# Kernel optimization log

Hardware: AMD Instinct MI355X
Metric: run time of the kernel (lower is better)

The kernel has to match this reference:

```python
import jax, jax.numpy as jnp
import numpy as np

B, T, D, H = 4, 2048, 1024, 16

def setup_inputs() -> dict:
    key = jax.random.key(0)
    ks = jax.random.split(key, 5)
    s = 1.0 / np.sqrt(D)
    return {
        "x":  jax.random.normal(ks[0], (B, T, D), dtype=jnp.float32),
        "Wq": jax.random.uniform(ks[1], (D, D), jnp.float32, -s, s),
        "Wk": jax.random.uniform(ks[2], (D, D), jnp.float32, -s, s),
        "Wv": jax.random.uniform(ks[3], (D, D), jnp.float32, -s, s),
        "Wo": jax.random.uniform(ks[4], (D, D), jnp.float32, -s, s),
    }

def reference(x, Wq, Wk, Wv, Wo):
    Bv, Tv, Dv = x.shape
    h = H
    k = Dv // h
    # Linear (no bias): y = x @ W.T, then split heads -> [B, h, T, k]
    Q = (x @ Wq.T).reshape(Bv, Tv, h, k).transpose(0, 2, 1, 3)
    K = (x @ Wk.T).reshape(Bv, Tv, h, k).transpose(0, 2, 1, 3)
    V = (x @ Wv.T).reshape(Bv, Tv, h, k).transpose(0, 2, 1, 3)
    scores = jnp.einsum('bhqk,bhsk->bhqs', Q, K) / jnp.sqrt(jnp.asarray(k, x.dtype))
    causal = jnp.tril(jnp.ones((Tv, Tv), dtype=bool))
    scores = jnp.where(causal[None, None], scores, jnp.asarray(-jnp.inf, x.dtype))
    A = jax.nn.softmax(scores, axis=-1)
    Y = jnp.einsum('bhqs,bhsk->bhqk', A, V).transpose(0, 2, 1, 3).reshape(Bv, Tv, Dv)
    return Y @ Wo.T
```

## Files before the change

kernel.cpp:

```cpp
#include <hip/hip_runtime.h>

typedef __attribute__((ext_vector_type(8))) short short8;
typedef __attribute__((ext_vector_type(4))) float f32x4;
typedef __attribute__((ext_vector_type(2))) unsigned int u32x2;

constexpr int B_ = 4, T_ = 2048, D_ = 1024, H_ = 16;
constexpr int M_ = B_ * T_;
constexpr float SCL2 = 0.1803368801111f;

#if __has_builtin(__builtin_amdgcn_exp2f)
#define EXP2F __builtin_amdgcn_exp2f
#else
#define EXP2F exp2f
#endif

#define DEV __device__ __forceinline__

DEV unsigned short f2bf(float f) {
  unsigned int u = __builtin_bit_cast(unsigned int, f);
  u += 0x7FFFu + ((u >> 16) & 1u);
  return (unsigned short)(u >> 16);
}

DEV void gload16(const unsigned short* g, unsigned short* l) {
  __builtin_amdgcn_global_load_lds(
      (const __attribute__((address_space(1))) unsigned int*)g,
      (__attribute__((address_space(3))) unsigned int*)l, 16, 0, 0);
}

__global__ __launch_bounds__(256) void cvt_bf16(const float* __restrict__ in,
                                                unsigned short* __restrict__ out,
                                                int n) {
  int i = (blockIdx.x * 256 + threadIdx.x) * 4;
  if (i >= n) return;
  float4 f = *(const float4*)(in + i);
  ushort4 o;
  o.x = f2bf(f.x); o.y = f2bf(f.y); o.z = f2bf(f.z); o.w = f2bf(f.w);
  *(ushort4*)(out + i) = o;
}

__global__ __launch_bounds__(256) void cvt_w4(const float* __restrict__ w0, const float* __restrict__ w1,
                                              const float* __restrict__ w2, const float* __restrict__ w3,
                                              unsigned short* __restrict__ o0, unsigned short* __restrict__ o1,
                                              unsigned short* __restrict__ o2, unsigned short* __restrict__ o3) {
  int sel = blockIdx.x >> 10;
  const float* in = sel == 0 ? w0 : sel == 1 ? w1 : sel == 2 ? w2 : w3;
  unsigned short* out = sel == 0 ? o0 : sel == 1 ? o1 : sel == 2 ? o2 : o3;
  int i = ((blockIdx.x & 1023) * 256 + threadIdx.x) * 4;
  float4 f = *(const float4*)(in + i);
  ushort4 o;
  o.x = f2bf(f.x); o.y = f2bf(f.y); o.z = f2bf(f.z); o.w = f2bf(f.w);
  *(ushort4*)(out + i) = o;
}

template <int OUTMODE>
__global__ __launch_bounds__(256, 2) void gemm_bt(const unsigned short* __restrict__ A,
                                                  const unsigned short* __restrict__ B,
                                                  void* __restrict__ C,
                                                  int M, int N, int K) {
  constexpr int BM = 128, BN = 128, BK = 64;
  __shared__ __align__(16) unsigned short a_sh[2 * BM * BK];
  __shared__ __align__(16) unsigned short b_sh[2 * BN * BK];

  const int tid = threadIdx.x;
  const int lane = tid & 63;
  const int w = tid >> 6;
  const int l15 = lane & 15, lg = lane >> 4;
  const int wr = w >> 1, wc = w & 1;

  const int nwg = gridDim.x;
  const int swz = (blockIdx.x & 7) * (nwg >> 3) + (blockIdx.x >> 3);

  const int NT = N / BN;
  const int tm = swz / NT, tn = swz % NT;
  const unsigned short* Ab = A + (size_t)tm * BM * K;
  const unsigned short* Bb = B + (size_t)tn * BN * K;

  f32x4 acc[4][4];
#pragma unroll
  for (int m = 0; m < 4; ++m)
#pragma unroll
    for (int n = 0; n < 4; ++n) acc[m][n] = (f32x4){0.f, 0.f, 0.f, 0.f};

  auto stage = [&](int buf, int kt) {
    int k0 = kt * BK;
#pragma unroll
    for (int rnd = 0; rnd < 4; ++rnd) {
      int c = rnd * 256 + tid;
      int row = c >> 3, s = c & 7;
      int koff = k0 + 8 * (s ^ (row & 7));
      unsigned short* ldst_a = a_sh + buf * BM * BK + (rnd * 256 + w * 64) * 8;
      unsigned short* ldst_b = b_sh + buf * BN * BK + (rnd * 256 + w * 64) * 8;
      gload16(Ab + (size_t)row * K + koff, ldst_a);
      gload16(Bb + (size_t)row * K + koff, ldst_b);
    }
  };

  stage(0, 0);
  int cur = 0;
  const int NK = K / BK;
  for (int kt = 0; kt < NK; ++kt) {
    __syncthreads();
    if (kt + 1 < NK) stage(cur ^ 1, kt + 1);
    const unsigned short* ab = a_sh + cur * BM * BK;
    const unsigned short* bb = b_sh + cur * BN * BK;
#pragma unroll
    for (int kk = 0; kk < 2; ++kk) {
      short8 af[4], bf8[4];
#pragma unroll
      for (int m = 0; m < 4; ++m) {
        int row = wr * 64 + m * 16 + l15;
        int slot = (kk * 4 + lg) ^ (row & 7);
        af[m] = *(const short8*)(ab + row * 64 + slot * 8);
      }
#pragma unroll
      for (int n = 0; n < 4; ++n) {
        int row = wc * 64 + n * 16 + l15;
        int slot = (kk * 4 + lg) ^ (row & 7);
        bf8[n] = *(const short8*)(bb + row * 64 + slot * 8);
      }
#pragma unroll
      for (int m = 0; m < 4; ++m)
#pragma unroll
        for (int n = 0; n < 4; ++n)
          acc[m][n] = __builtin_amdgcn_mfma_f32_16x16x32_bf16(af[m], bf8[n], acc[m][n], 0, 0, 0);
    }
    cur ^= 1;
  }

  const int row0 = tm * BM + wr * 64 + lg * 4;
  const int col0 = tn * BN + wc * 64 + l15;
#pragma unroll
  for (int m = 0; m < 4; ++m)
#pragma unroll
    for (int n = 0; n < 4; ++n) {
      if (OUTMODE == 3) {
        const int region = tn >> 3;
        const int nc = col0 - (region << 10) + n * 16;
        const int mm = row0 + m * 16;
        if (region == 2) {
          size_t base = (size_t)2 * 8388608 +
                        ((size_t)((mm >> 11) * 16 + (nc >> 6))) * 131072 +
                        (size_t)(nc & 63) * 2048 + (mm & 2047);
          ushort4 pk;
          pk.x = f2bf(acc[m][n][0]); pk.y = f2bf(acc[m][n][1]);
          pk.z = f2bf(acc[m][n][2]); pk.w = f2bf(acc[m][n][3]);
          *(ushort4*)((unsigned short*)C + base) = pk;
        } else {
          unsigned short* dst = (unsigned short*)C + (size_t)region * 8388608;
#pragma unroll
          for (int r = 0; r < 4; ++r)
            dst[(size_t)(mm + r) * 1024 + nc] = f2bf(acc[m][n][r]);
        }
      } else {
#pragma unroll
        for (int r = 0; r < 4; ++r) {
          size_t idx = (size_t)(row0 + m * 16 + r) * N + (col0 + n * 16);
          if (OUTMODE == 1)
            ((float*)C)[idx] = acc[m][n][r];
          else
            ((unsigned short*)C)[idx] = f2bf(acc[m][n][r]);
        }
      }
    }
}

__global__ __launch_bounds__(256, 3) void attn(const unsigned short* __restrict__ Q,
                                               const unsigned short* __restrict__ K,
                                               const unsigned short* __restrict__ Vt,
                                               unsigned short* __restrict__ Y) {
  __shared__ __align__(16) unsigned short k_sh[2][64 * 64];
  __shared__ __align__(16) unsigned short v_sh[2][64 * 64];
  __shared__ __align__(16) unsigned short p_sh[4][32][72];

  const int tid = threadIdx.x;
  const int lane = tid & 63;
  const int w = tid >> 6;
  const int l15 = lane & 15, lg = lane >> 4;

  const int bid = blockIdx.x;
  const int qt_blk = 15 - (bid >> 6);
  const int bh = bid & 63;
  const int h = bh & 15;
  const int b = bh >> 4;
  const int q0 = qt_blk * 128;
  const int qq0 = q0 + 32 * w;

  const unsigned short* Qp = Q + ((size_t)(b * T_ + q0)) * D_ + h * 64;
  const unsigned short* Kp = K + ((size_t)(b * T_)) * D_ + h * 64;
  const unsigned short* Vtp = Vt + (size_t)bh * 131072;

  auto stK = [&](int buf, int kv0) {
#pragma unroll
    for (int j = 0; j < 2; ++j) {
      int c = j * 256 + tid;
      int row = c >> 3;
      gload16(Kp + (size_t)(kv0 + row) * D_ + 8 * ((c & 7) ^ (row & 7)),
              &k_sh[buf][(j * 256 + w * 64) * 8]);
    }
  };
  auto stV = [&](int buf, int kv0) {
#pragma unroll
    for (int j = 0; j < 2; ++j) {
      int c = j * 256 + tid;
      int d = c >> 3;
      gload16(Vtp + (size_t)d * 2048 + kv0 + 8 * ((c & 7) ^ (d & 7)),
              &v_sh[buf][(j * 256 + w * 64) * 8]);
    }
  };

  short8 qf[2][2];
#pragma unroll
  for (int qt = 0; qt < 2; ++qt)
#pragma unroll
    for (int kk = 0; kk < 2; ++kk)
      qf[qt][kk] = *(const short8*)(Qp + (size_t)(32 * w + 16 * qt + l15) * D_ + 32 * kk + 8 * lg);

  stK(0, 0);
  stV(0, 0);
  __syncthreads();

  unsigned short* p_w = &p_sh[w][0][0];

  const float NEGINF = -__builtin_inff();
  float ml[2] = {NEGINF, NEGINF};
  float ll[2] = {0.f, 0.f};
  f32x4 o[2][4];
#pragma unroll
  for (int qt = 0; qt < 2; ++qt)
#pragma unroll
    for (int t = 0; t < 4; ++t) o[qt][t] = (f32x4){0.f, 0.f, 0.f, 0.f};

  const int NI = 2 * qt_blk + 2;
  int cur = 0;
  for (int i = 0; i < NI; ++i) {
    const int kv0 = i * 64;
    if (i + 1 < NI) { stK(cur ^ 1, kv0 + 64); stV(cur ^ 1, kv0 + 64); }

    const bool active = (kv0 <= qq0 + 31);
    if (active) {
      f32x4 sacc[2][4];
#pragma unroll
      for (int qt = 0; qt < 2; ++qt)
#pragma unroll
        for (int t = 0; t < 4; ++t) sacc[qt][t] = (f32x4){0.f, 0.f, 0.f, 0.f};
      const char* kb = (const char*)k_sh[cur];
      __builtin_amdgcn_s_setprio(1);
#pragma unroll
      for (int t = 0; t < 4; ++t) {
        int sr = 16 * t + l15;
        int sw = (sr & 7) << 4;
        short8 kf0 = *(const short8*)(kb + sr * 128 + ((16 * lg) ^ sw));
        short8 kf1 = *(const short8*)(kb + sr * 128 + ((64 + 16 * lg) ^ sw));
#pragma unroll
        for (int qt = 0; qt < 2; ++qt) {
          sacc[qt][t] = __builtin_amdgcn_mfma_f32_16x16x32_bf16(kf0, qf[qt][0], sacc[qt][t], 0, 0, 0);
          sacc[qt][t] = __builtin_amdgcn_mfma_f32_16x16x32_bf16(kf1, qf[qt][1], sacc[qt][t], 0, 0, 0);
        }
      }
      __builtin_amdgcn_s_setprio(0);

      float corr[2];
      bool defer[2];
#pragma unroll
      for (int qt = 0; qt < 2; ++qt) {
        const bool nomask = (kv0 + 63) <= (qq0 + 16 * qt);
        float sv[16];
        if (nomask) {
#pragma unroll
          for (int t = 0; t < 4; ++t)
#pragma unroll
            for (int r = 0; r < 4; ++r) sv[4 * t + r] = sacc[qt][t][r];
        } else {
          const int qg = qq0 + 16 * qt + l15;
#pragma unroll
          for (int t = 0; t < 4; ++t)
#pragma unroll
            for (int r = 0; r < 4; ++r) {
              int sg = kv0 + 16 * t + 4 * lg + r;
              sv[4 * t + r] = (sg <= qg) ? sacc[qt][t][r] : NEGINF;
            }
        }
        float a8[8], a4[4], a2[2];
#pragma unroll
        for (int k = 0; k < 8; ++k) a8[k] = fmaxf(sv[k], sv[k + 8]);
#pragma unroll
        for (int k = 0; k < 4; ++k) a4[k] = fmaxf(a8[k], a8[k + 4]);
        a2[0] = fmaxf(a4[0], a4[2]); a2[1] = fmaxf(a4[1], a4[3]);
        float mx = fmaxf(a2[0], a2[1]);
        mx = fmaxf(mx, __shfl_xor(mx, 16));
        mx = fmaxf(mx, __shfl_xor(mx, 32));
        defer[qt] = (__all(mx <= ml[qt] + 8.0f) != 0);
        float mnew = defer[qt] ? ml[qt] : fmaxf(ml[qt], mx);
        corr[qt] = defer[qt] ? 1.0f : EXP2F((ml[qt] - mnew) * SCL2);
        float nms2 = mnew * SCL2;
        float pv[16];
#pragma unroll
        for (int k = 0; k < 16; ++k) pv[k] = EXP2F(fmaf(sv[k], SCL2, -nms2));
        float s8[8], s4[4], s2[2];
#pragma unroll
        for (int k = 0; k < 8; ++k) s8[k] = pv[k] + pv[k + 8];
#pragma unroll
        for (int k = 0; k < 4; ++k) s4[k] = s8[k] + s8[k + 4];
        s2[0] = s4[0] + s4[2]; s2[1] = s4[1] + s4[3];
        float ps = s2[0] + s2[1];
        ps += __shfl_xor(ps, 16);
        ps += __shfl_xor(ps, 32);
        ll[qt] = ll[qt] * corr[qt] + ps;
        ml[qt] = mnew;
#pragma unroll
        for (int t = 0; t < 4; ++t) {
          unsigned lo, hi;
          asm("v_cvt_pk_bf16_f32 %0, %1, %2" : "=v"(lo) : "v"(pv[4 * t]), "v"(pv[4 * t + 1]));
          asm("v_cvt_pk_bf16_f32 %0, %1, %2" : "=v"(hi) : "v"(pv[4 * t + 2]), "v"(pv[4 * t + 3]));
          u32x2 pk = {lo, hi};
          *(u32x2*)(void*)(p_w + (16 * qt + l15) * 72 + 16 * t + 4 * lg) = pk;
        }
      }
      asm volatile("" ::: "memory");

#pragma unroll
      for (int qt = 0; qt < 2; ++qt)
        if (!defer[qt]) {
#pragma unroll
          for (int r = 0; r < 4; ++r) {
            float cr = __shfl(corr[qt], 4 * lg + r);
#pragma unroll
            for (int t = 0; t < 4; ++t) o[qt][t][r] *= cr;
          }
        }

      short8 pa[2][2];
#pragma unroll
      for (int qt = 0; qt < 2; ++qt)
#pragma unroll
        for (int kk = 0; kk < 2; ++kk)
          pa[qt][kk] = *(const short8*)(p_w + (16 * qt + l15) * 72 + kk * 32 + 8 * lg);

      const char* vbT = (const char*)v_sh[cur];
      __builtin_amdgcn_s_setprio(1);
#pragma unroll
      for (int t = 0; t < 4; ++t) {
        int dr = 16 * t + l15;
        int sw = (dr & 7) << 4;
        short8 vf0 = *(const short8*)(vbT + dr * 128 + ((16 * lg) ^ sw));
        short8 vf1 = *(const short8*)(vbT + dr * 128 + ((64 + 16 * lg) ^ sw));
#pragma unroll
        for (int qt = 0; qt < 2; ++qt) {
          o[qt][t] = __builtin_amdgcn_mfma_f32_16x16x32_bf16(pa[qt][0], vf0, o[qt][t], 0, 0, 0);
          o[qt][t] = __builtin_amdgcn_mfma_f32_16x16x32_bf16(pa[qt][1], vf1, o[qt][t], 0, 0, 0);
        }
      }
      __builtin_amdgcn_s_setprio(0);
    }
    __syncthreads();
    cur ^= 1;
  }

#pragma unroll
  for (int qt = 0; qt < 2; ++qt) {
    float linv = 1.0f / ll[qt];
#pragma unroll
    for (int r = 0; r < 4; ++r) {
      float li = __shfl(linv, 4 * lg + r);
      int qg = qq0 + 16 * qt + 4 * lg + r;
      unsigned short* Yp = Y + ((size_t)(b * T_ + qg)) * D_ + h * 64;
#pragma unroll
      for (int t = 0; t < 4; ++t)
        Yp[16 * t + l15] = f2bf(o[qt][t][r] * li);
    }
  }
}

extern "C" void kernel_launch(void* const* d_in, const int* in_sizes, int n_in,
                              void* d_out, int out_size, void* d_ws, size_t ws_size,
                              hipStream_t stream) {
  const float* x  = (const float*)d_in[0];
  const float* Wq = (const float*)d_in[1];
  const float* Wk = (const float*)d_in[2];
  const float* Wv = (const float*)d_in[3];
  const float* Wo = (const float*)d_in[4];
  float* out = (float*)d_out;

  const size_t NX = (size_t)M_ * D_;
  const size_t NW = (size_t)D_ * D_;
  const size_t need = (4 * NX + 4 * NW) * sizeof(unsigned short);
  if (ws_size < need) return;

  unsigned short* ws  = (unsigned short*)d_ws;
  unsigned short* xb  = ws;
  unsigned short* wqb = xb + NX;
  unsigned short* wkb = wqb + NW;
  unsigned short* wvb = wkb + NW;
  unsigned short* wob = wvb + NW;
  unsigned short* Qb  = wob + NW;
  unsigned short* Yb  = xb;

  cvt_bf16<<<(int)(NX / 1024), 256, 0, stream>>>(x, xb, (int)NX);
  cvt_w4<<<4096, 256, 0, stream>>>(Wq, Wk, Wv, Wo, wqb, wkb, wvb, wob);

  gemm_bt<3><<<(M_ / 128) * (3072 / 128), 256, 0, stream>>>(xb, wqb, Qb, M_, 3072, D_);

  attn<<<B_ * H_ * (T_ / 128), 256, 0, stream>>>(Qb, Qb + NX, Qb + 2 * NX, Yb);

  gemm_bt<1><<<(M_ / 128) * (D_ / 128), 256, 0, stream>>>(Yb, wob, out, M_, D_, D_);
}
```

Before: 167.2 us.

## Enlarge GEMM tile to 256x128 with 8 waves and ping-pong MFMA scheduling

The projection GEMMs move to a 256x128 tile computed by 512 threads (8 waves), with two K stages prefetched ahead and explicit vmcnt waits in place of a syncthreads before each stage. The MFMA work is split into four quadrant phases, each separated by s_barrier and setprio, so waves interleave LDS reads with matrix ops. The aim is more operand reuse per tile and better overlap of global loads with compute. In exchange it uses more LDS and registers per block, drops to one block per CU, and halves the grid size, so the tail and occupancy behaviour change.

```diff
diff --git a/kernel.cpp b/kernel.cpp
--- a/kernel.cpp
+++ b/kernel.cpp
@@ -54,11 +54,11 @@
 }
 
 template <int OUTMODE>
-__global__ __launch_bounds__(256, 2) void gemm_bt(const unsigned short* __restrict__ A,
+__global__ __launch_bounds__(512, 1) void gemm_bt(const unsigned short* __restrict__ A,
                                                   const unsigned short* __restrict__ B,
                                                   void* __restrict__ C,
                                                   int M, int N, int K) {
-  constexpr int BM = 128, BN = 128, BK = 64;
+  constexpr int BM = 256, BN = 128, BK = 64;
   __shared__ __align__(16) unsigned short a_sh[2 * BM * BK];
   __shared__ __align__(16) unsigned short b_sh[2 * BN * BK];
 
@@ -66,7 +66,8 @@
   const int lane = tid & 63;
   const int w = tid >> 6;
   const int l15 = lane & 15, lg = lane >> 4;
-  const int wr = w >> 1, wc = w & 1;
+  const int wr = w >> 1;
+  const int wc = w & 1;
 
   const int nwg = gridDim.x;
   const int swz = (blockIdx.x & 7) * (nwg >> 3) + (blockIdx.x >> 3);
@@ -82,50 +83,89 @@
 #pragma unroll
     for (int n = 0; n < 4; ++n) acc[m][n] = (f32x4){0.f, 0.f, 0.f, 0.f};
 
-  auto stage = [&](int buf, int kt) {
+  auto issue = [&](int buf, int kt) {
     int k0 = kt * BK;
 #pragma unroll
-    for (int rnd = 0; rnd < 4; ++rnd) {
-      int c = rnd * 256 + tid;
+    for (int r = 0; r < 4; ++r) {
+      int c = r * 512 + tid;
       int row = c >> 3, s = c & 7;
-      int koff = k0 + 8 * (s ^ (row & 7));
-      unsigned short* ldst_a = a_sh + buf * BM * BK + (rnd * 256 + w * 64) * 8;
-      unsigned short* ldst_b = b_sh + buf * BN * BK + (rnd * 256 + w * 64) * 8;
-      gload16(Ab + (size_t)row * K + koff, ldst_a);
-      gload16(Bb + (size_t)row * K + koff, ldst_b);
+      gload16(Ab + (size_t)row * K + k0 + 8 * (s ^ (row & 7)),
+              a_sh + buf * BM * BK + (r * 512 + w * 64) * 8);
+    }
+#pragma unroll
+    for (int r = 0; r < 2; ++r) {
+      int c = r * 512 + tid;
+      int row = c >> 3, s = c & 7;
+      gload16(Bb + (size_t)row * K + k0 + 8 * (s ^ (row & 7)),
+              b_sh + buf * BN * BK + (r * 512 + w * 64) * 8);
     }
   };
 
-  stage(0, 0);
-  int cur = 0;
   const int NK = K / BK;
+  issue(0, 0);
+  issue(1, 1);
+
   for (int kt = 0; kt < NK; ++kt) {
-    __syncthreads();
-    if (kt + 1 < NK) stage(cur ^ 1, kt + 1);
+    if (kt >= 1 && kt + 1 < NK) issue((kt + 1) & 1, kt + 1);
+    __builtin_amdgcn_sched_barrier(0);
+    if (kt + 1 < NK) asm volatile("s_waitcnt vmcnt(6)" ::: "memory");
+    else             asm volatile("s_waitcnt vmcnt(0)" ::: "memory");
+    __builtin_amdgcn_sched_barrier(0);
+    __builtin_amdgcn_s_barrier();
+    __builtin_amdgcn_sched_barrier(0);
+
+    const int cur = kt & 1;
     const unsigned short* ab = a_sh + cur * BM * BK;
     const unsigned short* bb = b_sh + cur * BN * BK;
-#pragma unroll
-    for (int kk = 0; kk < 2; ++kk) {
-      short8 af[4], bf8[4];
-#pragma unroll
-      for (int m = 0; m < 4; ++m) {
-        int row = wr * 64 + m * 16 + l15;
-        int slot = (kk * 4 + lg) ^ (row & 7);
-        af[m] = *(const short8*)(ab + row * 64 + slot * 8);
-      }
-#pragma unroll
-      for (int n = 0; n < 4; ++n) {
-        int row = wc * 64 + n * 16 + l15;
-        int slot = (kk * 4 + lg) ^ (row & 7);
-        bf8[n] = *(const short8*)(bb + row * 64 + slot * 8);
-      }
-#pragma unroll
-      for (int m = 0; m < 4; ++m)
-#pragma unroll
-        for (int n = 0; n < 4; ++n)
-          acc[m][n] = __builtin_amdgcn_mfma_f32_16x16x32_bf16(af[m], bf8[n], acc[m][n], 0, 0, 0);
-    }
-    cur ^= 1;
+    short8 af[4][2], bf[4][2];
+    auto rdA = [&](int m, int kk) {
+      int row = wr * 64 + m * 16 + l15;
+      int slot = (kk * 4 + lg) ^ (row & 7);
+      return *(const short8*)(ab + row * 64 + slot * 8);
+    };
+    auto rdB = [&](int n, int kk) {
+      int row = wc * 64 + n * 16 + l15;
+      int slot = (kk * 4 + lg) ^ (row & 7);
+      return *(const short8*)(bb + row * 64 + slot * 8);
+    };
+#define MM(m, n, kk) acc[m][n] = __builtin_amdgcn_mfma_f32_16x16x32_bf16(af[m][kk], bf[n][kk], acc[m][n], 0, 0, 0)
+
+    af[0][0] = rdA(0, 0); af[0][1] = rdA(0, 1);
+    af[1][0] = rdA(1, 0); af[1][1] = rdA(1, 1);
+    bf[0][0] = rdB(0, 0); bf[0][1] = rdB(0, 1);
+    bf[1][0] = rdB(1, 0); bf[1][1] = rdB(1, 1);
+    __builtin_amdgcn_s_setprio(1);
+    MM(0, 0, 0); MM(0, 0, 1); MM(0, 1, 0); MM(0, 1, 1);
+    MM(1, 0, 0); MM(1, 0, 1); MM(1, 1, 0); MM(1, 1, 1);
+    __builtin_amdgcn_s_setprio(0);
+    __builtin_amdgcn_s_barrier();
+    __builtin_amdgcn_sched_barrier(0);
+
+    af[2][0] = rdA(2, 0); af[2][1] = rdA(2, 1);
+    af[3][0] = rdA(3, 0); af[3][1] = rdA(3, 1);
+    __builtin_amdgcn_s_setprio(1);
+    MM(2, 0, 0); MM(2, 0, 1); MM(2, 1, 0); MM(2, 1, 1);
+    MM(3, 0, 0); MM(3, 0, 1); MM(3, 1, 0); MM(3, 1, 1);
+    __builtin_amdgcn_s_setprio(0);
+    __builtin_amdgcn_s_barrier();
+    __builtin_amdgcn_sched_barrier(0);
+
+    bf[2][0] = rdB(2, 0); bf[2][1] = rdB(2, 1);
+    bf[3][0] = rdB(3, 0); bf[3][1] = rdB(3, 1);
+    __builtin_amdgcn_s_setprio(1);
+    MM(2, 2, 0); MM(2, 2, 1); MM(2, 3, 0); MM(2, 3, 1);
+    MM(3, 2, 0); MM(3, 2, 1); MM(3, 3, 0); MM(3, 3, 1);
+    __builtin_amdgcn_s_setprio(0);
+    __builtin_amdgcn_s_barrier();
+    __builtin_amdgcn_sched_barrier(0);
+
+    __builtin_amdgcn_s_setprio(1);
+    MM(0, 2, 0); MM(0, 2, 1); MM(0, 3, 0); MM(0, 3, 1);
+    MM(1, 2, 0); MM(1, 2, 1); MM(1, 3, 0); MM(1, 3, 1);
+    __builtin_amdgcn_s_setprio(0);
+    __builtin_amdgcn_s_barrier();
+    __builtin_amdgcn_sched_barrier(0);
+#undef MM
   }
 
   const int row0 = tm * BM + wr * 64 + lg * 4;
@@ -399,9 +439,9 @@
   cvt_bf16<<<(int)(NX / 1024), 256, 0, stream>>>(x, xb, (int)NX);
   cvt_w4<<<4096, 256, 0, stream>>>(Wq, Wk, Wv, Wo, wqb, wkb, wvb, wob);
 
-  gemm_bt<3><<<(M_ / 128) * (3072 / 128), 256, 0, stream>>>(xb, wqb, Qb, M_, 3072, D_);
+  gemm_bt<3><<<(M_ / 256) * (3072 / 128), 512, 0, stream>>>(xb, wqb, Qb, M_, 3072, D_);
 
   attn<<<B_ * H_ * (T_ / 128), 256, 0, stream>>>(Qb, Qb + NX, Qb + 2 * NX, Yb);
 
-  gemm_bt<1><<<(M_ / 128) * (D_ / 128), 256, 0, stream>>>(Yb, wob, out, M_, D_, D_);
-}
+  gemm_bt<1><<<(M_ / 256) * (D_ / 128), 512, 0, stream>>>(Yb, wob, out, M_, D_, D_);
+}
```

New measurement: 185.0 us. +10.6%, slower.
